# Kernel tuning notes

Measured on AMD Instinct MI355X. Metric: run time of the kernel, lower is better.

The kernel has to match this reference:

```python
import jax, jax.numpy as jnp
import numpy as np

D = 128
N_AUTHOR = 100000
N_PAPER = 200000
N_LAYERS = 2


def setup_inputs() -> dict:
    key = jax.random.key(0)
    ks = jax.random.split(key, 16)
    inp = {
        "x_author": jax.random.normal(ks[0], (N_AUTHOR, D), dtype=jnp.float32),
        "x_paper": jax.random.normal(ks[1], (N_PAPER, D), dtype=jnp.float32),
        "edge_index": jax.random.randint(ks[2], (2, 500000), 0, 100000, dtype=jnp.int32),
        "coauthor_edge_index": jax.random.randint(ks[3], (2, 250000), 0, 100000, dtype=jnp.int32),
        "supervision_edge_index": jax.random.randint(ks[4], (2, 100000), 0, 100000, dtype=jnp.int32),
    }
    scale = 1.0 / np.sqrt(D)
    names = ["W_a2p", "W_p2a", "W_aself", "W_pself", "W_co"]
    for i, n in enumerate(names):
        inp[n] = jax.random.uniform(ks[5 + i], (N_LAYERS, D, D), jnp.float32, -scale, scale)
        inp["b" + n[1:]] = jax.random.uniform(ks[10 + i], (N_LAYERS, D), jnp.float32, -scale, scale)
    return inp


def _linear(x, W, b):
    # torch.nn.Linear: y = x @ W.T + b
    return x @ W.T + b


def reference(x_author, x_paper, edge_index, coauthor_edge_index, supervision_edge_index,
              W_a2p, b_a2p, W_p2a, b_p2a, W_aself, b_aself, W_pself, b_pself, W_co, b_co):
    author_idx, paper_idx = edge_index[0], edge_index[1]
    co_src, co_dst = coauthor_edge_index[0], coauthor_edge_index[1]
    for l in range(N_LAYERS):
        # author -> paper messages
        msg_a = _linear(x_author[author_idx], W_a2p[l], b_a2p[l])       # [E, D]
        agg_to_papers = jax.ops.segment_sum(msg_a, paper_idx, num_segments=x_paper.shape[0])
        # paper -> author messages
        msg_p = _linear(x_paper[paper_idx], W_p2a[l], b_p2a[l])         # [E, D]
        agg_to_authors = jax.ops.segment_sum(msg_p, author_idx, num_segments=x_author.shape[0])
        x_paper = agg_to_papers + _linear(x_paper, W_pself[l], b_pself[l])
        x_author = agg_to_authors + _linear(x_author, W_aself[l], b_aself[l])
        # coauthor edges (author -> author)
        msg_co = _linear(x_author[co_src], W_co[l], b_co[l])            # [E_co, D]
        agg_co = jax.ops.segment_sum(msg_co, co_dst, num_segments=x_author.shape[0])
        x_author = x_author + agg_co
    a = x_author[supervision_edge_index[0]]
    p = x_paper[supervision_edge_index[1]]
    return (a * p).sum(axis=1)
```

## Files before the change

kernel.cpp:

```cpp
#include <hip/hip_runtime.h>

#define DD 128
#define ADJ_CAP 1024

typedef __attribute__((ext_vector_type(8))) short short8;
typedef __attribute__((ext_vector_type(4))) float f32x4;

__device__ inline unsigned short f2bf(float f) {
    unsigned u = __float_as_uint(f);
    unsigned r = (u + 0x7fffu + ((u >> 16) & 1u)) >> 16;
    return (unsigned short)r;
}
__device__ inline float bf2f(unsigned short u) {
    return __uint_as_float(((unsigned)u) << 16);
}
__device__ inline float bflo(unsigned u) { return __uint_as_float(u << 16); }
__device__ inline float bfhi(unsigned u) { return __uint_as_float(u & 0xffff0000u); }
__device__ inline unsigned pack2(float a, float b) {
    return (unsigned)f2bf(a) | ((unsigned)f2bf(b) << 16);
}

__global__ __launch_bounds__(256) void conv_all(const float* __restrict__ inA, unsigned short* __restrict__ outA, int n4A,
                                                const float* __restrict__ inP, unsigned short* __restrict__ outP, int n4P) {
    int i = blockIdx.x * blockDim.x + threadIdx.x;
    const float* in;
    unsigned short* out;
    int j;
    if (i < n4A) { in = inA; out = outA; j = i; }
    else if (i < n4A + n4P) { in = inP; out = outP; j = i - n4A; }
    else return;
    float4 v = *(const float4*)(in + (size_t)j * 4);
    uint2 o;
    o.x = pack2(v.x, v.y);
    o.y = pack2(v.z, v.w);
    *(uint2*)(out + (size_t)j * 4) = o;
}

__global__ __launch_bounds__(256) void pack_all(const float* __restrict__ Wa2p, const float* __restrict__ Wpself,
                                                const float* __restrict__ Wp2a, const float* __restrict__ Waself,
                                                const float* __restrict__ Wco,
                                                short* __restrict__ BPp0, short* __restrict__ BPp1,
                                                short* __restrict__ BPa0, short* __restrict__ BPa1,
                                                short* __restrict__ BPc0, short* __restrict__ BPc1) {
    const int WL = 128 * 128;
    int idx = blockIdx.x * blockDim.x + threadIdx.x;
    int seg = idx >> 12;
    int sidx = idx & 4095;
    const float *W1, *W2;
    short* dst;
    int ktiles;
    switch (seg) {
        case 0: W1 = Wa2p;      W2 = Wpself;      dst = BPp0; ktiles = 8; break;
        case 1: W1 = Wa2p + WL; W2 = Wpself + WL; dst = BPp1; ktiles = 8; break;
        case 2: W1 = Wp2a;      W2 = Waself;      dst = BPa0; ktiles = 8; break;
        case 3: W1 = Wp2a + WL; W2 = Waself + WL; dst = BPa1; ktiles = 8; break;
        case 4: W1 = Wco;       W2 = nullptr;     dst = BPc0; ktiles = 4; break;
        default: W1 = Wco + WL; W2 = nullptr;     dst = BPc1; ktiles = 4; break;
    }
    int total = 8 * ktiles * 64;
    if (sidx >= total) return;
    int lane = sidx & 63;
    int kk = (sidx >> 6) % ktiles;
    int t = (sidx >> 6) / ktiles;
    int n = t * 16 + (lane & 15);
    int kbase = kk * 32 + (lane >> 4) * 8;
    short8 v;
#pragma unroll
    for (int j = 0; j < 8; ++j) {
        int k = kbase + j;
        float f = (k < 128) ? W1[n * 128 + k] : W2[n * 128 + (k - 128)];
        v[j] = (short)f2bf(f);
    }
    *(short8*)(dst + (size_t)sidx * 8) = v;
}

__global__ __launch_bounds__(256) void count_all(const int* __restrict__ aidx, const int* __restrict__ pidx,
                                                 const int* __restrict__ cod,
                                                 int* __restrict__ cntP, int* __restrict__ cntA,
                                                 int* __restrict__ cntC, int E, int Eco) {
    int i = blockIdx.x * blockDim.x + threadIdx.x;
    if (i < E) {
        atomicAdd(&cntP[pidx[i]], 1);
        atomicAdd(&cntA[aidx[i]], 1);
    } else if (i < E + Eco) {
        atomicAdd(&cntC[cod[i - E]], 1);
    }
}

__global__ __launch_bounds__(256) void scan_local3(const int* __restrict__ c0, int* __restrict__ r0, int* __restrict__ p0, int N0,
                                                   const int* __restrict__ c1, int* __restrict__ r1, int* __restrict__ p1, int N1,
                                                   const int* __restrict__ c2, int* __restrict__ r2, int* __restrict__ p2, int N2,
                                                   int nb0, int nb1) {
    __shared__ int sh[256];
    int b = blockIdx.x;
    const int* cnt; int* row; int* partials; int N; int lb;
    if (b < nb0) { cnt = c0; row = r0; partials = p0; N = N0; lb = b; }
    else if (b < nb0 + nb1) { cnt = c1; row = r1; partials = p1; N = N1; lb = b - nb0; }
    else { cnt = c2; row = r2; partials = p2; N = N2; lb = b - nb0 - nb1; }
    int t = threadIdx.x;
    int base = lb * 1024 + t * 4;
    int v0 = 0, v1 = 0, v2 = 0, v3 = 0;
    if (base + 0 < N) v0 = cnt[base + 0];
    if (base + 1 < N) v1 = cnt[base + 1];
    if (base + 2 < N) v2 = cnt[base + 2];
    if (base + 3 < N) v3 = cnt[base + 3];
    sh[t] = v0 + v1 + v2 + v3;
    __syncthreads();
    for (int off = 1; off < 256; off <<= 1) {
        int y = (t >= off) ? sh[t - off] : 0;
        __syncthreads();
        sh[t] += y;
        __syncthreads();
    }
    int excl = (t > 0) ? sh[t - 1] : 0;
    if (t == 255) partials[lb] = sh[255];
    if (base + 0 < N) row[base + 0] = excl; excl += v0;
    if (base + 1 < N) row[base + 1] = excl; excl += v1;
    if (base + 2 < N) row[base + 2] = excl; excl += v2;
    if (base + 3 < N) row[base + 3] = excl;
}

__global__ __launch_bounds__(256) void scan_partials3(int* __restrict__ p0, int nb0,
                                                      int* __restrict__ p1, int nb1,
                                                      int* __restrict__ p2, int nb2) {
    __shared__ int sh[256];
    int* partials; int nb;
    if (blockIdx.x == 0) { partials = p0; nb = nb0; }
    else if (blockIdx.x == 1) { partials = p1; nb = nb1; }
    else { partials = p2; nb = nb2; }
    int t = threadIdx.x;
    int v = (t < nb) ? partials[t] : 0;
    sh[t] = v;
    __syncthreads();
    for (int off = 1; off < 256; off <<= 1) {
        int y = (t >= off) ? sh[t - off] : 0;
        __syncthreads();
        sh[t] += y;
        __syncthreads();
    }
    if (t < nb) partials[t] = (t > 0) ? sh[t - 1] : 0;
}

__global__ __launch_bounds__(256) void scan_finalize3(int* __restrict__ r0, int* __restrict__ cu0, const int* __restrict__ p0, int N0,
                                                      int* __restrict__ r1, int* __restrict__ cu1, const int* __restrict__ p1, int N1,
                                                      int* __restrict__ r2, int* __restrict__ cu2, const int* __restrict__ p2, int N2,
                                                      int fb0, int fb1) {
    int b = blockIdx.x;
    int* row; int* cur; const int* partials; int N; int lb;
    if (b < fb0) { row = r0; cur = cu0; partials = p0; N = N0; lb = b; }
    else if (b < fb0 + fb1) { row = r1; cur = cu1; partials = p1; N = N1; lb = b - fb0; }
    else { row = r2; cur = cu2; partials = p2; N = N2; lb = b - fb0 - fb1; }
    int i = lb * 256 + threadIdx.x;
    if (i >= N) return;
    int r = row[i] + partials[i >> 10];
    row[i] = r;
    cur[i] = r;
}

__global__ __launch_bounds__(256) void fill_all(const int* __restrict__ aidx, const int* __restrict__ pidx,
                                                const int* __restrict__ cos_, const int* __restrict__ cod,
                                                int* __restrict__ curP, int* __restrict__ curA, int* __restrict__ curC,
                                                int* __restrict__ adjP, int* __restrict__ adjA, int* __restrict__ adjC,
                                                int E, int Eco) {
    int i = blockIdx.x * blockDim.x + threadIdx.x;
    if (i < E) {
        int a = aidx[i], pp = pidx[i];
        adjP[atomicAdd(&curP[pp], 1)] = a;
        adjA[atomicAdd(&curA[a], 1)] = pp;
    } else if (i < E + Eco) {
        adjC[atomicAdd(&curC[cod[i - E]], 1)] = cos_[i - E];
    }
}

struct FParams {
    const unsigned short* gsrc;
    const unsigned short* selfx;
    const unsigned short* base;
    const int* adj;
    const int* rowp;
    const int* cnt;
    const short* Bpack;
    const float* b1;
    const float* b2;
    unsigned short* out;
    int M;
};

template <int KTILES, bool HAS_B2, bool ADD_BASE>
__device__ __forceinline__ void fused_body(char* lds, int* ldsAdj, const FParams& p, int blk) {
    const int tid = threadIdx.x;
    const int node0 = blk * 64;
    const int grp = tid >> 4;
    const int l = tid & 15;

    const int lastNode = (node0 + 63 < p.M) ? node0 + 63 : p.M - 1;
    const int est = p.rowp[node0];
    const int eend = p.rowp[lastNode] + p.cnt[lastNode];
    const int nE = eend - est;
    for (int j = tid; j < nE && j < ADJ_CAP; j += 256) ldsAdj[j] = p.adj[est + j];

    int relSt[4], dA[4];
#pragma unroll
    for (int i = 0; i < 4; ++i) {
        int node = node0 + grp * 4 + i;
        bool ok = node < p.M;
        relSt[i] = ok ? (p.rowp[node] - est) : 0;
        dA[i] = ok ? p.cnt[node] : 0;
    }
    __syncthreads();

    float acc[4][8];
#pragma unroll
    for (int i = 0; i < 4; ++i)
#pragma unroll
        for (int j = 0; j < 8; ++j) acc[i][j] = 0.f;

    int dmax = dA[0];
#pragma unroll
    for (int i = 1; i < 4; ++i) dmax = dA[i] > dmax ? dA[i] : dmax;

    auto gather = [&](auto idxAt) {
        for (int k = 0; k < dmax; k += 4) {
#pragma unroll
            for (int i = 0; i < 4; ++i) {
                if (k < dA[i]) {
                    int rem = dA[i] - k;
                    int o0 = relSt[i] + k;
                    int s0 = idxAt(o0);
                    int s1 = idxAt(o0 + ((rem > 1) ? 1 : 0));
                    int s2 = idxAt(o0 + ((rem > 2) ? 2 : 0));
                    int s3 = idxAt(o0 + ((rem > 3) ? 3 : 0));
                    float w1 = (rem > 1) ? 1.f : 0.f;
                    float w2 = (rem > 2) ? 1.f : 0.f;
                    float w3 = (rem > 3) ? 1.f : 0.f;
                    uint4 v0 = *(const uint4*)(p.gsrc + (size_t)s0 * DD + l * 8);
                    uint4 v1 = *(const uint4*)(p.gsrc + (size_t)s1 * DD + l * 8);
                    uint4 v2 = *(const uint4*)(p.gsrc + (size_t)s2 * DD + l * 8);
                    uint4 v3 = *(const uint4*)(p.gsrc + (size_t)s3 * DD + l * 8);
                    acc[i][0] += bflo(v0.x); acc[i][1] += bfhi(v0.x);
                    acc[i][2] += bflo(v0.y); acc[i][3] += bfhi(v0.y);
                    acc[i][4] += bflo(v0.z); acc[i][5] += bfhi(v0.z);
                    acc[i][6] += bflo(v0.w); acc[i][7] += bfhi(v0.w);
                    acc[i][0] += w1 * bflo(v1.x); acc[i][1] += w1 * bfhi(v1.x);
                    acc[i][2] += w1 * bflo(v1.y); acc[i][3] += w1 * bfhi(v1.y);
                    acc[i][4] += w1 * bflo(v1.z); acc[i][5] += w1 * bfhi(v1.z);
                    acc[i][6] += w1 * bflo(v1.w); acc[i][7] += w1 * bfhi(v1.w);
                    acc[i][0] += w2 * bflo(v2.x); acc[i][1] += w2 * bfhi(v2.x);
                    acc[i][2] += w2 * bflo(v2.y); acc[i][3] += w2 * bfhi(v2.y);
                    acc[i][4] += w2 * bflo(v2.z); acc[i][5] += w2 * bfhi(v2.z);
                    acc[i][6] += w2 * bflo(v2.w); acc[i][7] += w2 * bfhi(v2.w);
                    acc[i][0] += w3 * bflo(v3.x); acc[i][1] += w3 * bfhi(v3.x);
                    acc[i][2] += w3 * bflo(v3.y); acc[i][3] += w3 * bfhi(v3.y);
                    acc[i][4] += w3 * bflo(v3.z); acc[i][5] += w3 * bfhi(v3.z);
                    acc[i][6] += w3 * bflo(v3.w); acc[i][7] += w3 * bfhi(v3.w);
                }
            }
        }
    };
    if (nE <= ADJ_CAP) gather([&](int o) { return ldsAdj[o]; });
    else               gather([&](int o) { return p.adj[est + o]; });

#pragma unroll
    for (int i = 0; i < 4; ++i) {
        int lr = grp * 4 + i;
        uint4 o = make_uint4(pack2(acc[i][0], acc[i][1]), pack2(acc[i][2], acc[i][3]),
                             pack2(acc[i][4], acc[i][5]), pack2(acc[i][6], acc[i][7]));
        int colb = l * 16;
        *(uint4*)(lds + lr * 256 + (colb ^ ((lr & 7) << 4))) = o;
    }
    __syncthreads();

    const int wave = tid >> 6;
    const int lane = tid & 63;
    const int kg = lane >> 4;
    const int lrA = wave * 16 + (lane & 15);

    f32x4 facc[8];
#pragma unroll
    for (int t = 0; t < 8; ++t) facc[t] = (f32x4){0.f, 0.f, 0.f, 0.f};

#pragma unroll
    for (int kk = 0; kk < 4; ++kk) {
        int colb = kk * 64 + kg * 16;
        short8 af = *(const short8*)(lds + lrA * 256 + (colb ^ ((lrA & 7) << 4)));
#pragma unroll
        for (int t = 0; t < 8; ++t) {
            short8 bf = *(const short8*)(p.Bpack + ((size_t)(t * KTILES + kk) * 64 + lane) * 8);
            facc[t] = __builtin_amdgcn_mfma_f32_16x16x32_bf16(af, bf, facc[t], 0, 0, 0);
        }
    }
    if (KTILES == 8) {
        int srow = node0 + wave * 16 + (lane & 15);
        if (srow >= p.M) srow = p.M - 1;
        const unsigned short* sp = p.selfx + (size_t)srow * DD + kg * 8;
#pragma unroll
        for (int kk = 4; kk < 8; ++kk) {
            short8 af = *(const short8*)(sp + (kk - 4) * 32);
#pragma unroll
            for (int t = 0; t < 8; ++t) {
                short8 bf = *(const short8*)(p.Bpack + ((size_t)(t * 8 + kk) * 64 + lane) * 8);
                facc[t] = __builtin_amdgcn_mfma_f32_16x16x32_bf16(af, bf, facc[t], 0, 0, 0);
            }
        }
    }

    const int col0 = lane & 15;
    const int crow0 = node0 + wave * 16 + kg * 4;
#pragma unroll
    for (int t = 0; t < 8; ++t) {
        int col = t * 16 + col0;
        float bb = p.b1[col];
        float b2v = HAS_B2 ? p.b2[col] : 0.f;
#pragma unroll
        for (int r = 0; r < 4; ++r) {
            int row = crow0 + r;
            if (row < p.M) {
                float v = facc[t][r] + (float)p.cnt[row] * bb + b2v;
                if (ADD_BASE) v += bf2f(p.base[(size_t)row * DD + col]);
                p.out[(size_t)row * DD + col] = f2bf(v);
            }
        }
    }
}

__global__ __launch_bounds__(256, 6) void fused_dual_kernel(FParams pP, FParams pA, int blkP) {
    __shared__ char lds[16384];
    __shared__ int ldsAdj[ADJ_CAP];
    bool isP = (int)blockIdx.x < blkP;
    const FParams& p = isP ? pP : pA;
    fused_body<8, true, false>(lds, ldsAdj, p, isP ? blockIdx.x : blockIdx.x - blkP);
}

__global__ __launch_bounds__(256, 6) void fused_co_kernel(FParams p) {
    __shared__ char lds[16384];
    __shared__ int ldsAdj[ADJ_CAP];
    fused_body<4, false, true>(lds, ldsAdj, p, blockIdx.x);
}

__global__ __launch_bounds__(256) void dot_kernel(
    const unsigned short* __restrict__ xa, const unsigned short* __restrict__ xp,
    const int* __restrict__ s0, const int* __restrict__ s1,
    float* __restrict__ out, int E) {
    int g = blockIdx.x * blockDim.x + threadIdx.x;
    int e = g >> 4;
    int l = g & 15;
    if (e >= E) return;
    int a = s0[e], p = s1[e];
    uint4 va = *(const uint4*)(xa + (size_t)a * DD + l * 8);
    uint4 vp = *(const uint4*)(xp + (size_t)p * DD + l * 8);
    float s = bflo(va.x) * bflo(vp.x) + bfhi(va.x) * bfhi(vp.x)
            + bflo(va.y) * bflo(vp.y) + bfhi(va.y) * bfhi(vp.y)
            + bflo(va.z) * bflo(vp.z) + bfhi(va.z) * bfhi(vp.z)
            + bflo(va.w) * bflo(vp.w) + bfhi(va.w) * bfhi(vp.w);
    s += __shfl_xor(s, 1); s += __shfl_xor(s, 2);
    s += __shfl_xor(s, 4); s += __shfl_xor(s, 8);
    if (l == 0) out[e] = s;
}

extern "C" void kernel_launch(void* const* d_in, const int* in_sizes, int n_in,
                              void* d_out, int out_size, void* d_ws, size_t ws_size,
                              hipStream_t stream) {
    const float* xa_in = (const float*)d_in[0];
    const float* xp_in = (const float*)d_in[1];
    const int* eidx = (const int*)d_in[2];
    const int* co = (const int*)d_in[3];
    const int* sup = (const int*)d_in[4];
    const float* W_a2p = (const float*)d_in[5];
    const float* b_a2p = (const float*)d_in[6];
    const float* W_p2a = (const float*)d_in[7];
    const float* b_p2a = (const float*)d_in[8];
    const float* W_aself = (const float*)d_in[9];
    const float* b_aself = (const float*)d_in[10];
    const float* W_pself = (const float*)d_in[11];
    const float* b_pself = (const float*)d_in[12];
    const float* W_co = (const float*)d_in[13];
    const float* b_co = (const float*)d_in[14];

    const int NA = in_sizes[0] / DD;
    const int NP = in_sizes[1] / DD;
    const int E = in_sizes[2] / 2;
    const int Eco = in_sizes[3] / 2;
    const int Esup = in_sizes[4] / 2;
    const int* a_idx = eidx;
    const int* p_idx = eidx + E;
    const int* co_s = co;
    const int* co_d = co + Eco;
    const int* s0 = sup;
    const int* s1 = sup + Esup;

    char* w = (char*)d_ws;
    auto carve = [&](size_t bytes) -> char* {
        char* p = w;
        w += (bytes + 255) & ~(size_t)255;
        return p;
    };
    unsigned short* XA = (unsigned short*)carve((size_t)NA * DD * 2);
    unsigned short* XP = (unsigned short*)carve((size_t)NP * DD * 2);
    unsigned short* P0b = (unsigned short*)carve((size_t)NP * DD * 2);
    unsigned short* P1b = (unsigned short*)carve((size_t)NP * DD * 2);
    unsigned short* A0b = (unsigned short*)carve((size_t)NA * DD * 2);
    unsigned short* A1b = (unsigned short*)carve((size_t)NA * DD * 2);
    int* cntP = (int*)carve((size_t)NP * 4);
    int* cntA = (int*)carve((size_t)NA * 4);
    int* cntC = (int*)carve((size_t)NA * 4);
    size_t cntSpan = (size_t)((char*)cntC - (char*)cntP) + (((size_t)NA * 4 + 255) & ~(size_t)255);
    int* rowP = (int*)carve((size_t)NP * 4);
    int* curP = (int*)carve((size_t)NP * 4);
    int* rowA = (int*)carve((size_t)NA * 4);
    int* curA = (int*)carve((size_t)NA * 4);
    int* rowC = (int*)carve((size_t)NA * 4);
    int* curC = (int*)carve((size_t)NA * 4);
    int* adjP = (int*)carve((size_t)E * 4);
    int* adjA = (int*)carve((size_t)E * 4);
    int* adjC = (int*)carve((size_t)Eco * 4);
    int* partP = (int*)carve(256 * 4);
    int* partA = (int*)carve(256 * 4);
    int* partC = (int*)carve(256 * 4);
    short* BPp0 = (short*)carve(8 * 8 * 64 * 8 * 2);
    short* BPp1 = (short*)carve(8 * 8 * 64 * 8 * 2);
    short* BPa0 = (short*)carve(8 * 8 * 64 * 8 * 2);
    short* BPa1 = (short*)carve(8 * 8 * 64 * 8 * 2);
    short* BPc0 = (short*)carve(8 * 4 * 64 * 8 * 2);
    short* BPc1 = (short*)carve(8 * 4 * 64 * 8 * 2);

    int n4A = NA * DD / 4, n4P = NP * DD / 4;
    conv_all<<<(n4A + n4P + 255) / 256, 256, 0, stream>>>(xa_in, XA, n4A, xp_in, XP, n4P);
    pack_all<<<96, 256, 0, stream>>>(W_a2p, W_pself, W_p2a, W_aself, W_co, BPp0, BPp1, BPa0, BPa1, BPc0, BPc1);

    hipMemsetAsync(cntP, 0, cntSpan, stream);
    count_all<<<(E + Eco + 255) / 256, 256, 0, stream>>>(a_idx, p_idx, co_d, cntP, cntA, cntC, E, Eco);
    const int nbP = (NP + 1023) / 1024;
    const int nbA = (NA + 1023) / 1024;
    scan_local3<<<nbP + nbA + nbA, 256, 0, stream>>>(cntP, rowP, partP, NP, cntA, rowA, partA, NA, cntC, rowC, partC, NA, nbP, nbA);
    scan_partials3<<<3, 256, 0, stream>>>(partP, nbP, partA, nbA, partC, nbA);
    const int fbP = (NP + 255) / 256;
    const int fbA = (NA + 255) / 256;
    scan_finalize3<<<fbP + fbA + fbA, 256, 0, stream>>>(rowP, curP, partP, NP, rowA, curA, partA, NA, rowC, curC, partC, NA, fbP, fbA);
    fill_all<<<(E + Eco + 255) / 256, 256, 0, stream>>>(a_idx, p_idx, co_s, co_d, curP, curA, curC, adjP, adjA, adjC, E, Eco);

    const int blkP = (NP + 63) / 64;
    const int blkA = (NA + 63) / 64;

    FParams pP1 = {XA, XP, nullptr, adjP, rowP, cntP, BPp0, b_a2p, b_pself, P0b, NP};
    FParams pA1 = {XP, XA, nullptr, adjA, rowA, cntA, BPa0, b_p2a, b_aself, A0b, NA};
    FParams pC1 = {A0b, nullptr, A0b, adjC, rowC, cntC, BPc0, b_co, nullptr, A1b, NA};
    FParams pP2 = {A1b, P0b, nullptr, adjP, rowP, cntP, BPp1, b_a2p + 128, b_pself + 128, P1b, NP};
    FParams pA2 = {P0b, A1b, nullptr, adjA, rowA, cntA, BPa1, b_p2a + 128, b_aself + 128, A0b, NA};
    FParams pC2 = {A0b, nullptr, A0b, adjC, rowC, cntC, BPc1, b_co + 128, nullptr, A1b, NA};

    fused_dual_kernel<<<blkP + blkA, 256, 0, stream>>>(pP1, pA1, blkP);
    fused_co_kernel<<<blkA, 256, 0, stream>>>(pC1);
    fused_dual_kernel<<<blkP + blkA, 256, 0, stream>>>(pP2, pA2, blkP);
    fused_co_kernel<<<blkA, 256, 0, stream>>>(pC2);

    dot_kernel<<<(Esup * 16 + 255) / 256, 256, 0, stream>>>(A1b, P1b, s0, s1, (float*)d_out, Esup);
}
```

Measured before the change: 534.1 us.

## Switch fused GEMM to 32x32x16 MFMA with per-wave column tiles

The dense part of the fused gather+linear kernel moves from 16x16x32 MFMA, where each wave owned 16 rows and all 128 columns, to 32x32x16 MFMA, where each wave owns 32 output columns across all 64 rows. The weight pack layout and LDS swizzle are rewritten to match, and occupancy bounds drop from 6 to 5 blocks. The aim is fewer weight-fragment loads per MFMA and better matrix-unit efficiency. The cost is larger accumulators (two f32x16 per lane), lower occupancy, and each wave now reading the self-feature rows itself.

```diff
diff --git a/kernel.cpp b/kernel.cpp
--- a/kernel.cpp
+++ b/kernel.cpp
@@ -4,7 +4,7 @@
 #define ADJ_CAP 1024
 
 typedef __attribute__((ext_vector_type(8))) short short8;
-typedef __attribute__((ext_vector_type(4))) float f32x4;
+typedef __attribute__((ext_vector_type(16))) float f32x16;
 
 __device__ inline unsigned short f2bf(float f) {
     unsigned u = __float_as_uint(f);
@@ -48,22 +48,23 @@
     int sidx = idx & 4095;
     const float *W1, *W2;
     short* dst;
-    int ktiles;
+    int KS;
     switch (seg) {
-        case 0: W1 = Wa2p;      W2 = Wpself;      dst = BPp0; ktiles = 8; break;
-        case 1: W1 = Wa2p + WL; W2 = Wpself + WL; dst = BPp1; ktiles = 8; break;
-        case 2: W1 = Wp2a;      W2 = Waself;      dst = BPa0; ktiles = 8; break;
-        case 3: W1 = Wp2a + WL; W2 = Waself + WL; dst = BPa1; ktiles = 8; break;
-        case 4: W1 = Wco;       W2 = nullptr;     dst = BPc0; ktiles = 4; break;
-        default: W1 = Wco + WL; W2 = nullptr;     dst = BPc1; ktiles = 4; break;
-    }
-    int total = 8 * ktiles * 64;
+        case 0: W1 = Wa2p;      W2 = Wpself;      dst = BPp0; KS = 16; break;
+        case 1: W1 = Wa2p + WL; W2 = Wpself + WL; dst = BPp1; KS = 16; break;
+        case 2: W1 = Wp2a;      W2 = Waself;      dst = BPa0; KS = 16; break;
+        case 3: W1 = Wp2a + WL; W2 = Waself + WL; dst = BPa1; KS = 16; break;
+        case 4: W1 = Wco;       W2 = nullptr;     dst = BPc0; KS = 8; break;
+        default: W1 = Wco + WL; W2 = nullptr;     dst = BPc1; KS = 8; break;
+    }
+    int total = 4 * KS * 64;
     if (sidx >= total) return;
     int lane = sidx & 63;
-    int kk = (sidx >> 6) % ktiles;
-    int t = (sidx >> 6) / ktiles;
-    int n = t * 16 + (lane & 15);
-    int kbase = kk * 32 + (lane >> 4) * 8;
+    int rest = sidx >> 6;
+    int ks = rest % KS;
+    int ct = rest / KS;
+    int n = ct * 32 + (lane & 31);
+    int kbase = ks * 16 + (lane >> 5) * 8;
     short8 v;
 #pragma unroll
     for (int j = 0; j < 8; ++j) {
@@ -186,7 +187,7 @@
     int M;
 };
 
-template <int KTILES, bool HAS_B2, bool ADD_BASE>
+template <int KS, bool HAS_B2, bool ADD_BASE>
 __device__ __forceinline__ void fused_body(char* lds, int* ldsAdj, const FParams& p, int blk) {
     const int tid = threadIdx.x;
     const int node0 = blk * 64;
@@ -266,75 +267,79 @@
         uint4 o = make_uint4(pack2(acc[i][0], acc[i][1]), pack2(acc[i][2], acc[i][3]),
                              pack2(acc[i][4], acc[i][5]), pack2(acc[i][6], acc[i][7]));
         int colb = l * 16;
-        *(uint4*)(lds + lr * 256 + (colb ^ ((lr & 7) << 4))) = o;
+        *(uint4*)(lds + lr * 256 + (colb ^ ((lr & 15) << 4))) = o;
     }
     __syncthreads();
 
     const int wave = tid >> 6;
     const int lane = tid & 63;
-    const int kg = lane >> 4;
-    const int lrA = wave * 16 + (lane & 15);
-
-    f32x4 facc[8];
-#pragma unroll
-    for (int t = 0; t < 8; ++t) facc[t] = (f32x4){0.f, 0.f, 0.f, 0.f};
-
-#pragma unroll
-    for (int kk = 0; kk < 4; ++kk) {
-        int colb = kk * 64 + kg * 16;
-        short8 af = *(const short8*)(lds + lrA * 256 + (colb ^ ((lrA & 7) << 4)));
-#pragma unroll
-        for (int t = 0; t < 8; ++t) {
-            short8 bf = *(const short8*)(p.Bpack + ((size_t)(t * KTILES + kk) * 64 + lane) * 8);
-            facc[t] = __builtin_amdgcn_mfma_f32_16x16x32_bf16(af, bf, facc[t], 0, 0, 0);
+    const int l5 = lane >> 5;
+    const int l31 = lane & 31;
+    const short* bp = p.Bpack + (size_t)wave * KS * 64 * 8;
+
+    f32x16 acc0 = {0.f, 0.f, 0.f, 0.f, 0.f, 0.f, 0.f, 0.f, 0.f, 0.f, 0.f, 0.f, 0.f, 0.f, 0.f, 0.f};
+    f32x16 acc1 = acc0;
+
+    int sr0 = node0 + l31;      if (sr0 >= p.M) sr0 = p.M - 1;
+    int sr1 = node0 + 32 + l31; if (sr1 >= p.M) sr1 = p.M - 1;
+    const int r0 = l31, r1 = 32 + l31;
+
+#pragma unroll
+    for (int ks = 0; ks < KS; ++ks) {
+        short8 bf = *(const short8*)(bp + ((size_t)ks * 64 + lane) * 8);
+        short8 a0, a1;
+        if (ks < 8) {
+            int colb = ks * 32 + l5 * 16;
+            a0 = *(const short8*)(lds + r0 * 256 + (colb ^ ((r0 & 15) << 4)));
+            a1 = *(const short8*)(lds + r1 * 256 + (colb ^ ((r1 & 15) << 4)));
+        } else {
+            int off = (ks - 8) * 16 + l5 * 8;
+            a0 = *(const short8*)(p.selfx + (size_t)sr0 * DD + off);
+            a1 = *(const short8*)(p.selfx + (size_t)sr1 * DD + off);
         }
-    }
-    if (KTILES == 8) {
-        int srow = node0 + wave * 16 + (lane & 15);
-        if (srow >= p.M) srow = p.M - 1;
-        const unsigned short* sp = p.selfx + (size_t)srow * DD + kg * 8;
-#pragma unroll
-        for (int kk = 4; kk < 8; ++kk) {
-            short8 af = *(const short8*)(sp + (kk - 4) * 32);
-#pragma unroll
-            for (int t = 0; t < 8; ++t) {
-                short8 bf = *(const short8*)(p.Bpack + ((size_t)(t * 8 + kk) * 64 + lane) * 8);
-                facc[t] = __builtin_amdgcn_mfma_f32_16x16x32_bf16(af, bf, facc[t], 0, 0, 0);
-            }
-        }
-    }
-
-    const int col0 = lane & 15;
-    const int crow0 = node0 + wave * 16 + kg * 4;
-#pragma unroll
-    for (int t = 0; t < 8; ++t) {
-        int col = t * 16 + col0;
-        float bb = p.b1[col];
-        float b2v = HAS_B2 ? p.b2[col] : 0.f;
-#pragma unroll
-        for (int r = 0; r < 4; ++r) {
-            int row = crow0 + r;
+        acc0 = __builtin_amdgcn_mfma_f32_32x32x16_bf16(a0, bf, acc0, 0, 0, 0);
+        acc1 = __builtin_amdgcn_mfma_f32_32x32x16_bf16(a1, bf, acc1, 0, 0, 0);
+    }
+
+    const int col = wave * 32 + l31;
+    const float bb = p.b1[col];
+    const float b2v = HAS_B2 ? p.b2[col] : 0.f;
+    {
+        int rb = node0 + 4 * l5;
+#pragma unroll
+        for (int g = 0; g < 16; ++g) {
+            int row = rb + (g & 3) + 8 * (g >> 2);
             if (row < p.M) {
-                float v = facc[t][r] + (float)p.cnt[row] * bb + b2v;
+                float v = acc0[g] + (float)p.cnt[row] * bb + b2v;
                 if (ADD_BASE) v += bf2f(p.base[(size_t)row * DD + col]);
                 p.out[(size_t)row * DD + col] = f2bf(v);
             }
         }
-    }
-}
-
-__global__ __launch_bounds__(256, 6) void fused_dual_kernel(FParams pP, FParams pA, int blkP) {
+        rb += 32;
+#pragma unroll
+        for (int g = 0; g < 16; ++g) {
+            int row = rb + (g & 3) + 8 * (g >> 2);
+            if (row < p.M) {
+                float v = acc1[g] + (float)p.cnt[row] * bb + b2v;
+                if (ADD_BASE) v += bf2f(p.base[(size_t)row * DD + col]);
+                p.out[(size_t)row * DD + col] = f2bf(v);
+            }
+        }
+    }
+}
+
+__global__ __launch_bounds__(256, 5) void fused_dual_kernel(FParams pP, FParams pA, int blkP) {
     __shared__ char lds[16384];
     __shared__ int ldsAdj[ADJ_CAP];
     bool isP = (int)blockIdx.x < blkP;
     const FParams& p = isP ? pP : pA;
-    fused_body<8, true, false>(lds, ldsAdj, p, isP ? blockIdx.x : blockIdx.x - blkP);
-}
-
-__global__ __launch_bounds__(256, 6) void fused_co_kernel(FParams p) {
+    fused_body<16, true, false>(lds, ldsAdj, p, isP ? blockIdx.x : blockIdx.x - blkP);
+}
+
+__global__ __launch_bounds__(256, 5) void fused_co_kernel(FParams p) {
     __shared__ char lds[16384];
     __shared__ int ldsAdj[ADJ_CAP];
-    fused_body<4, false, true>(lds, ldsAdj, p, blockIdx.x);
+    fused_body<8, false, true>(lds, ldsAdj, p, blockIdx.x);
 }
 
 __global__ __launch_bounds__(256) void dot_kernel(
@@ -416,12 +421,12 @@
     int* partP = (int*)carve(256 * 4);
     int* partA = (int*)carve(256 * 4);
     int* partC = (int*)carve(256 * 4);
-    short* BPp0 = (short*)carve(8 * 8 * 64 * 8 * 2);
-    short* BPp1 = (short*)carve(8 * 8 * 64 * 8 * 2);
-    short* BPa0 = (short*)carve(8 * 8 * 64 * 8 * 2);
-    short* BPa1 = (short*)carve(8 * 8 * 64 * 8 * 2);
-    short* BPc0 = (short*)carve(8 * 4 * 64 * 8 * 2);
-    short* BPc1 = (short*)carve(8 * 4 * 64 * 8 * 2);
+    short* BPp0 = (short*)carve(4 * 16 * 64 * 8 * 2);
+    short* BPp1 = (short*)carve(4 * 16 * 64 * 8 * 2);
+    short* BPa0 = (short*)carve(4 * 16 * 64 * 8 * 2);
+    short* BPa1 = (short*)carve(4 * 16 * 64 * 8 * 2);
+    short* BPc0 = (short*)carve(4 * 8 * 64 * 8 * 2);
+    short* BPc1 = (short*)carve(4 * 8 * 64 * 8 * 2);
 
     int n4A = NA * DD / 4, n4P = NP * DD / 4;
     conv_all<<<(n4A + n4P + 255) / 256, 256, 0, stream>>>(xa_in, XA, n4A, xp_in, XP, n4P);
```

After: 500.9 us. 1.07x faster.
